# Performance work log

Measured on AMD Instinct MI355X. Metric: run time of the kernel, lower is better.

Reference implementation:

```python
import jax, jax.numpy as jnp
import numpy as np

D = 1024
DFF = 4096
B, S = 4, 2048
EPS = 1e-6
SLOPE = 0.01  # torch LeakyReLU default


def setup_inputs() -> dict:
    key = jax.random.key(0)
    ks = jax.random.split(key, 16)
    sd = 1.0 / np.sqrt(D)
    sf = 1.0 / np.sqrt(DFF)
    return {
        "X": jax.random.normal(ks[0], (B, S, D), dtype=jnp.float32),
        "intensity": jax.random.uniform(ks[1], (B, S, S), dtype=jnp.float32),
        "Wq": jax.random.uniform(ks[2], (D, D), jnp.float32, -sd, sd),
        "bq": jax.random.uniform(ks[3], (D,), jnp.float32, -sd, sd),
        "Wk": jax.random.uniform(ks[4], (D, D), jnp.float32, -sd, sd),
        "bk": jax.random.uniform(ks[5], (D,), jnp.float32, -sd, sd),
        "Wv": jax.random.uniform(ks[6], (D, D), jnp.float32, -sd, sd),
        "bv": jax.random.uniform(ks[7], (D,), jnp.float32, -sd, sd),
        "Wo": jax.random.uniform(ks[8], (D, D), jnp.float32, -sd, sd),
        "bo": jax.random.uniform(ks[9], (D,), jnp.float32, -sd, sd),
        "W1": jax.random.uniform(ks[10], (D, DFF), jnp.float32, -sd, sd),
        "b1": jax.random.uniform(ks[11], (DFF,), jnp.float32, -sd, sd),
        "W2": jax.random.uniform(ks[12], (DFF, D), jnp.float32, -sf, sf),
        "b2": jax.random.uniform(ks[13], (D,), jnp.float32, -sf, sf),
        "g1": jnp.ones((D,), jnp.float32),
        "be1": jnp.zeros((D,), jnp.float32),
        "g2": jnp.ones((D,), jnp.float32),
        "be2": jnp.zeros((D,), jnp.float32),
    }


def _layernorm(x, g, b):
    mu = jnp.mean(x, axis=-1, keepdims=True)
    var = jnp.mean(jnp.square(x - mu), axis=-1, keepdims=True)
    return (x - mu) * jax.lax.rsqrt(var + EPS) * g + b


def reference(X, intensity, Wq, bq, Wk, bk, Wv, bv, Wo, bo, W1, b1, W2, b2, g1, be1, g2, be2):
    d_k = X.shape[-1]
    q = X @ Wq + bq
    k = X @ Wk + bk
    v = X @ Wv + bv
    # scores: [B,S,S]; scale applied to k^T as in source
    scores = jnp.einsum('bid,bjd->bij', q, k) / jnp.sqrt(jnp.float32(d_k))
    attn = jax.nn.softmax(scores, axis=-1) + intensity  # post-softmax bias add
    out = jnp.einsum('bij,bjd->bid', attn, v) @ Wo + bo
    h = _layernorm(out + X, g1, be1)
    ffn = jax.nn.leaky_relu(h @ W1 + b1, negative_slope=SLOPE) @ W2 + b2
    return _layernorm(ffn + h, g2, be2)
```

## Files before the change

### kernel.cpp

```cpp
#include <hip/hip_runtime.h>

#define B_   4
#define S_   2048
#define D_   1024
#define DFF_ 4096

typedef __attribute__((ext_vector_type(8))) short short8;
typedef __attribute__((ext_vector_type(4))) float floatx4;

__device__ __forceinline__ unsigned short f2b(float f) {
    unsigned int u = __float_as_uint(f);
    unsigned int r = (u + 0x7fffu + ((u >> 16) & 1u)) >> 16;
    return (unsigned short)r;
}
__device__ __forceinline__ float b2f(unsigned short u) {
    return __uint_as_float((unsigned int)u << 16);
}

__device__ __forceinline__ void swizzle_xy(int gx, int gy, int& bx, int& by) {
    if ((gy & 7) == 0) {
        const int linear = by * gx + bx;
        const int xcd = linear & 7;
        const int slot = linear >> 3;
        const int r = slot / gx;
        by = xcd * (gy >> 3) + r;
        bx = slot - r * gx;
    }
}

#define GLL(src, dst) __builtin_amdgcn_global_load_lds( \
    (const __attribute__((address_space(1))) void*)(src), \
    (__attribute__((address_space(3))) void*)(dst), 16, 0, 0)

__device__ __forceinline__ void barrier_mem() {
    asm volatile("" ::: "memory");
    __builtin_amdgcn_s_barrier();
    asm volatile("" ::: "memory");
}

__device__ __forceinline__ void gemm_core256sq(
    const unsigned short* __restrict__ A,
    const unsigned short* __restrict__ Bt,
    int ldA, int ldB, int K, int m0, int n0,
    unsigned short* __restrict__ lds,
    floatx4 acc[8][4])
{
    const int tid  = threadIdx.x;
    const int lane = tid & 63;
    const int wave = tid >> 6;
    const int wm   = wave >> 2;
    const int wn   = wave & 3;

    const int ra = tid >> 3;
    const int pg = tid & 7;
    const int cg = (pg ^ (ra & 7)) * 8;
    const unsigned short* gA = A  + (long long)(m0 + ra) * ldA + cg;
    const unsigned short* gB = Bt + (long long)(n0 + ra) * ldB + cg;
    const long long rsA = 64LL * ldA;
    const long long rsB = 64LL * ldB;
    unsigned short* const sAbase = lds + wave * 512;
    unsigned short* const sBbase = lds + 32768 + wave * 512;

    const int fr = lane & 15;
    const int q  = lane >> 4;
    const int sw0 = (q ^ (fr & 7)) * 8;
    const int sw1 = sw0 ^ 32;
    const unsigned short* const pA = lds + (wm * 128 + fr) * 64;
    const unsigned short* const pB = lds + 32768 + (wn * 64 + fr) * 64;

    short8 Af[4][2];
    short8 Bf[2][2][2];

#define STG_A(buf, h, kk) do { \
    const unsigned short* _s = gA + (long long)(h) * 2 * rsA + (kk); \
    unsigned short* _d = sAbase + (buf) * 16384 + (h) * 8192; \
    GLL(_s, _d); GLL(_s + rsA, _d + 4096); } while (0)
#define STG_B(buf, h, kk) do { \
    const unsigned short* _s = gB + (long long)(h) * 2 * rsB + (kk); \
    unsigned short* _d = sBbase + (buf) * 16384 + (h) * 8192; \
    GLL(_s, _d); GLL(_s + rsB, _d + 4096); } while (0)
#define LD_A(bufo, mh) do { \
    _Pragma("unroll") for (int _i = 0; _i < 4; ++_i) { \
        Af[_i][0] = *(const short8*)(pA + (bufo) + (mh) * 4096 + _i * 1024 + sw0); \
        Af[_i][1] = *(const short8*)(pA + (bufo) + (mh) * 4096 + _i * 1024 + sw1); } } while (0)
#define LD_B(bufo, np) do { \
    _Pragma("unroll") for (int _j = 0; _j < 2; ++_j) { \
        Bf[np][_j][0] = *(const short8*)(pB + (bufo) + (np) * 2048 + _j * 1024 + sw0); \
        Bf[np][_j][1] = *(const short8*)(pB + (bufo) + (np) * 2048 + _j * 1024 + sw1); } } while (0)
#define MM(mh, np) do { \
    _Pragma("unroll") for (int _i = 0; _i < 4; ++_i) \
    _Pragma("unroll") for (int _j = 0; _j < 2; ++_j) \
    _Pragma("unroll") for (int _h = 0; _h < 2; ++_h) \
        acc[(mh) * 4 + _i][(np) * 2 + _j] = __builtin_amdgcn_mfma_f32_16x16x32_bf16( \
            Af[_i][_h], Bf[np][_j][_h], acc[(mh) * 4 + _i][(np) * 2 + _j], 0, 0, 0); \
    } while (0)
#define PRIO1() __builtin_amdgcn_s_setprio(1)
#define PRIO0() __builtin_amdgcn_s_setprio(0)
#define VMC(n)  asm volatile("s_waitcnt vmcnt(" #n ")" ::: "memory")

    const int NT = K >> 6;
    const long long kcap = (long long)K - 64;

    STG_B(0, 0, 0); STG_B(0, 1, 0);
    STG_A(0, 0, 0); STG_A(0, 1, 0);
    STG_B(1, 0, 64); STG_B(1, 1, 64);
    VMC(4);
    barrier_mem();

    for (int t = 0; t < NT; t += 2) {
        const long long k1 = (long long)(t + 1) * 64;
        long long k2 = (long long)(t + 2) * 64; if (k2 > kcap) k2 = kcap;
        long long k3 = (long long)(t + 3) * 64; if (k3 > kcap) k3 = kcap;

        STG_A(1, 0, k1); STG_A(1, 1, k1);
        LD_A(0, 0); LD_B(0, 0); LD_B(0, 1);
        PRIO1(); MM(0, 0); MM(0, 1); PRIO0();
        barrier_mem();
        STG_B(0, 0, k2); STG_B(0, 1, k2);
        LD_A(0, 1);
        PRIO1(); MM(1, 0); MM(1, 1); PRIO0();
        VMC(4);
        barrier_mem();
        STG_A(0, 0, k2); STG_A(0, 1, k2);
        LD_A(16384, 0); LD_B(16384, 0); LD_B(16384, 1);
        PRIO1(); MM(0, 0); MM(0, 1); PRIO0();
        barrier_mem();
        STG_B(1, 0, k3); STG_B(1, 1, k3);
        LD_A(16384, 1);
        PRIO1(); MM(1, 0); MM(1, 1); PRIO0();
        VMC(4);
        barrier_mem();
    }
    VMC(0);

#undef STG_A
#undef STG_B
#undef LD_A
#undef LD_B
#undef MM
#undef PRIO1
#undef PRIO0
#undef VMC
}

__global__ __launch_bounds__(256) void cast_bf16_kernel(
    const float4* __restrict__ src, ushort4* __restrict__ dst, int n4)
{
    int i = blockIdx.x * 256 + threadIdx.x;
    if (i < n4) {
        float4 f = src[i];
        ushort4 u;
        u.x = f2b(f.x); u.y = f2b(f.y); u.z = f2b(f.z); u.w = f2b(f.w);
        dst[i] = u;
    }
}

__global__ __launch_bounds__(256) void transpose_cast_kernel(
    const float* __restrict__ W, unsigned short* __restrict__ Wt, int K, int N)
{
    __shared__ float tile[32][33];
    const int tx = threadIdx.x;
    const int ty = threadIdx.y;
    const int bx = blockIdx.x * 32;
    const int by = blockIdx.y * 32;
#pragma unroll
    for (int j = 0; j < 32; j += 8)
        tile[ty + j][tx] = W[(long long)(by + ty + j) * N + bx + tx];
    __syncthreads();
#pragma unroll
    for (int j = 0; j < 32; j += 8)
        Wt[(long long)(bx + ty + j) * K + by + tx] = f2b(tile[tx][ty + j]);
}

__global__ __launch_bounds__(256) void vtrans_kernel(
    const unsigned short* __restrict__ Vb, unsigned short* __restrict__ Vt)
{
    __shared__ unsigned short tile[64][68];
    const int b  = blockIdx.z;
    const int s0 = blockIdx.y * 64;
    const int d0 = blockIdx.x * 64;
    const int tx = threadIdx.x & 15;
    const int ty = threadIdx.x >> 4;

    const unsigned short* src = Vb + ((long long)b * S_ + s0) * D_ + d0;
#pragma unroll
    for (int j = 0; j < 4; j++) {
        const int s = j * 16 + ty;
        ushort4 v = *(const ushort4*)(src + (long long)s * D_ + tx * 4);
        tile[tx * 4 + 0][s] = v.x;
        tile[tx * 4 + 1][s] = v.y;
        tile[tx * 4 + 2][s] = v.z;
        tile[tx * 4 + 3][s] = v.w;
    }
    __syncthreads();
    unsigned short* dst = Vt + ((long long)b * D_ + d0) * S_ + s0;
#pragma unroll
    for (int j = 0; j < 4; j++) {
        const int d = j * 16 + ty;
        ushort4 v;
        v.x = tile[d][tx * 4 + 0];
        v.y = tile[d][tx * 4 + 1];
        v.z = tile[d][tx * 4 + 2];
        v.w = tile[d][tx * 4 + 3];
        *(ushort4*)(dst + (long long)d * S_ + tx * 4) = v;
    }
}

template <int OUT_BF16, int ACT_LEAKY, int HAS_BIAS>
__global__ __launch_bounds__(512, 2) void gemm_bt(
    const unsigned short* __restrict__ A,
    const unsigned short* __restrict__ Bt,
    void* __restrict__ Cptr,
    const float* __restrict__ bias,
    int M, int N, int K, float scale,
    long long sA, long long sB, long long sC)
{
    __shared__ unsigned short lds[65536];

    const int lane = threadIdx.x & 63;
    const int wave = threadIdx.x >> 6;
    const int z    = blockIdx.z;

    int bx = blockIdx.x, by = blockIdx.y;
    swizzle_xy(gridDim.x, gridDim.y, bx, by);
    const int m0 = by * 256;
    const int n0 = bx * 256;

    floatx4 acc[8][4];
#pragma unroll
    for (int i = 0; i < 8; i++)
#pragma unroll
        for (int j = 0; j < 4; j++) acc[i][j] = floatx4{0.f, 0.f, 0.f, 0.f};

    gemm_core256sq(A + (long long)z * sA, Bt + (long long)z * sB,
                   K, K, K, m0, n0, lds, acc);

    const int wr = (wave >> 2) * 128;
    const int wc = (wave & 3) * 64;
    const int cr = (lane >> 4) * 4;
    const int cc = lane & 15;
    float* Cf = (float*)Cptr;
    unsigned short* Cb = (unsigned short*)Cptr;

#pragma unroll
    for (int mi = 0; mi < 8; mi++) {
#pragma unroll
        for (int ni = 0; ni < 4; ni++) {
            const int col = n0 + wc + ni * 16 + cc;
            const float bv = HAS_BIAS ? bias[col] : 0.0f;
#pragma unroll
            for (int r = 0; r < 4; r++) {
                const int row = m0 + wr + mi * 16 + cr + r;
                float v = acc[mi][ni][r] * scale + bv;
                if (ACT_LEAKY) v = (v > 0.0f) ? v : 0.01f * v;
                const long long idx = (long long)z * sC + (long long)row * N + col;
                if (OUT_BF16) Cb[idx] = f2b(v); else Cf[idx] = v;
            }
        }
    }
}

template <int NK>
__global__ __launch_bounds__(512, 2) void gemm_bt_sk(
    const unsigned short* __restrict__ A,
    const unsigned short* __restrict__ Bt,
    unsigned short* __restrict__ P,
    int M, int N, int Kslice, int ldA, int ldB,
    long long sA, long long sB)
{
    __shared__ unsigned short lds[65536];

    const int lane = threadIdx.x & 63;
    const int wave = threadIdx.x >> 6;
    const int z    = blockIdx.z;
    const int ks   = z % NK;
    const int b    = z / NK;
    const int nb   = gridDim.z / NK;

    int bx = blockIdx.x, by = blockIdx.y;
    swizzle_xy(gridDim.x, gridDim.y, bx, by);
    const int m0 = by * 256;
    const int n0 = bx * 256;

    floatx4 acc[8][4];
#pragma unroll
    for (int i = 0; i < 8; i++)
#pragma unroll
        for (int j = 0; j < 4; j++) acc[i][j] = floatx4{0.f, 0.f, 0.f, 0.f};

    gemm_core256sq(A + (long long)b * sA + (long long)ks * Kslice,
                   Bt + (long long)b * sB + (long long)ks * Kslice,
                   ldA, ldB, Kslice, m0, n0, lds, acc);

    const long long pbase = ((long long)ks * nb + b) * (long long)M * N;

    const int wr = (wave >> 2) * 128;
    const int wc = (wave & 3) * 64;
    const int cr = (lane >> 4) * 4;
    const int cc = lane & 15;

#pragma unroll
    for (int mi = 0; mi < 8; mi++) {
#pragma unroll
        for (int ni = 0; ni < 4; ni++) {
            const int col = n0 + wc + ni * 16 + cc;
#pragma unroll
            for (int r = 0; r < 4; r++) {
                const int row = m0 + wr + mi * 16 + cr + r;
                P[pbase + (long long)row * N + col] = f2b(acc[mi][ni][r]);
            }
        }
    }
}

__global__ __launch_bounds__(512, 2) void gemm_qkv(
    const unsigned short* __restrict__ A,
    const unsigned short* __restrict__ Bt,
    unsigned short* __restrict__ Qb,
    unsigned short* __restrict__ Kb,
    unsigned short* __restrict__ Vb,
    const float* __restrict__ bq,
    const float* __restrict__ bk,
    const float* __restrict__ bv)
{
    __shared__ unsigned short lds[65536];

    const int lane = threadIdx.x & 63;
    const int wave = threadIdx.x >> 6;

    int bx = blockIdx.x, by = blockIdx.y;
    swizzle_xy(gridDim.x, gridDim.y, bx, by);
    const int m0 = by * 256;
    const int n0 = bx * 256;

    floatx4 acc[8][4];
#pragma unroll
    for (int i = 0; i < 8; i++)
#pragma unroll
        for (int j = 0; j < 4; j++) acc[i][j] = floatx4{0.f, 0.f, 0.f, 0.f};

    gemm_core256sq(A, Bt, D_, D_, D_, m0, n0, lds, acc);

    const int wr = (wave >> 2) * 128;
    const int wc = (wave & 3) * 64;
    const int cr = (lane >> 4) * 4;
    const int cc = lane & 15;

#pragma unroll
    for (int mi = 0; mi < 8; mi++) {
#pragma unroll
        for (int ni = 0; ni < 4; ni++) {
            const int col = n0 + wc + ni * 16 + cc;
            const int seg = col >> 10;
            const int c = col & 1023;
            const float* bp = (seg == 0) ? bq : ((seg == 1) ? bk : bv);
            unsigned short* dp = (seg == 0) ? Qb : ((seg == 1) ? Kb : Vb);
            const float bval = bp[c];
#pragma unroll
            for (int r = 0; r < 4; r++) {
                const int row = m0 + wr + mi * 16 + cr + r;
                dp[(long long)row * D_ + c] = f2b(acc[mi][ni][r] + bval);
            }
        }
    }
}

__global__ __launch_bounds__(256) void avred_kernel(
    const ushort4* __restrict__ p0, const ushort4* __restrict__ p1,
    ushort4* __restrict__ dst, int n4)
{
    int i = blockIdx.x * 256 + threadIdx.x;
    if (i < n4) {
        ushort4 a = p0[i], b = p1[i];
        ushort4 u;
        u.x = f2b(b2f(a.x) + b2f(b.x)); u.y = f2b(b2f(a.y) + b2f(b.y));
        u.z = f2b(b2f(a.z) + b2f(b.z)); u.w = f2b(b2f(a.w) + b2f(b.w));
        dst[i] = u;
    }
}

template <int HAS_OUTB>
__global__ __launch_bounds__(256) void ln_red_kernel(
    const unsigned short* __restrict__ p0, const unsigned short* __restrict__ p1,
    const float* __restrict__ resid, const float* __restrict__ bias,
    const float* __restrict__ g, const float* __restrict__ b,
    float* __restrict__ out_f, unsigned short* __restrict__ out_b)
{
    __shared__ float red[8];
    const long long row = blockIdx.x;
    const int tid = threadIdx.x;
    const ushort4 a0 = ((const ushort4*)(p0 + row * D_))[tid];
    const ushort4 a1 = ((const ushort4*)(p1 + row * D_))[tid];
    const float4 rv = ((const float4*)(resid + row * D_))[tid];
    const float4 bi = ((const float4*)bias)[tid];
    float v0 = b2f(a0.x) + b2f(a1.x) + bi.x + rv.x;
    float v1 = b2f(a0.y) + b2f(a1.y) + bi.y + rv.y;
    float v2 = b2f(a0.z) + b2f(a1.z) + bi.z + rv.z;
    float v3 = b2f(a0.w) + b2f(a1.w) + bi.w + rv.w;

    float s = v0 + v1 + v2 + v3;
#pragma unroll
    for (int o = 32; o > 0; o >>= 1) s += __shfl_xor(s, o);
    if ((tid & 63) == 0) red[tid >> 6] = s;
    __syncthreads();
    const float mean = (red[0] + red[1] + red[2] + red[3]) * (1.0f / D_);

    const float d0 = v0 - mean, d1 = v1 - mean, d2 = v2 - mean, d3 = v3 - mean;
    float qv = d0 * d0 + d1 * d1 + d2 * d2 + d3 * d3;
#pragma unroll
    for (int o = 32; o > 0; o >>= 1) qv += __shfl_xor(qv, o);
    if ((tid & 63) == 0) red[4 + (tid >> 6)] = qv;
    __syncthreads();
    const float var = (red[4] + red[5] + red[6] + red[7]) * (1.0f / D_);
    const float inv = rsqrtf(var + 1e-6f);

    const float4 gv = ((const float4*)g)[tid];
    const float4 bv = ((const float4*)b)[tid];
    const float o0 = d0 * inv * gv.x + bv.x;
    const float o1 = d1 * inv * gv.y + bv.y;
    const float o2 = d2 * inv * gv.z + bv.z;
    const float o3 = d3 * inv * gv.w + bv.w;

    ((float4*)(out_f + row * D_))[tid] = float4{o0, o1, o2, o3};
    if (HAS_OUTB) {
        ushort4 u; u.x = f2b(o0); u.y = f2b(o1); u.z = f2b(o2); u.w = f2b(o3);
        ((ushort4*)(out_b + row * D_))[tid] = u;
    }
}

__global__ __launch_bounds__(256) void softmax_bias_kernel(
    const unsigned short* __restrict__ scores, const float* __restrict__ intensity,
    unsigned short* __restrict__ attn)
{
    __shared__ float red[8];
    const long long row = blockIdx.x;
    const int tid = threadIdx.x;
    const ushort4* s4 = (const ushort4*)(scores + row * S_);
    const float4* i4 = (const float4*)(intensity + row * S_);
    ushort4* dst = (ushort4*)(attn + row * S_);

    float vv[8];
    {
        ushort4 a = s4[tid], b = s4[tid + 256];
        vv[0] = b2f(a.x); vv[1] = b2f(a.y); vv[2] = b2f(a.z); vv[3] = b2f(a.w);
        vv[4] = b2f(b.x); vv[5] = b2f(b.y); vv[6] = b2f(b.z); vv[7] = b2f(b.w);
    }

    float mx = vv[0];
#pragma unroll
    for (int i = 1; i < 8; i++) mx = fmaxf(mx, vv[i]);
#pragma unroll
    for (int o = 32; o > 0; o >>= 1) mx = fmaxf(mx, __shfl_xor(mx, o));
    if ((tid & 63) == 0) red[tid >> 6] = mx;
    __syncthreads();
    mx = fmaxf(fmaxf(red[0], red[1]), fmaxf(red[2], red[3]));

    float e[8];
    float sum = 0.f;
#pragma unroll
    for (int i = 0; i < 8; i++) { e[i] = __expf(vv[i] - mx); sum += e[i]; }
#pragma unroll
    for (int o = 32; o > 0; o >>= 1) sum += __shfl_xor(sum, o);
    if ((tid & 63) == 0) red[4 + (tid >> 6)] = sum;
    __syncthreads();
    sum = red[4] + red[5] + red[6] + red[7];
    const float rs = 1.0f / sum;

#pragma unroll
    for (int i = 0; i < 2; i++) {
        float4 iv = i4[tid + 256 * i];
        ushort4 o;
        o.x = f2b(e[4 * i + 0] * rs + iv.x);
        o.y = f2b(e[4 * i + 1] * rs + iv.y);
        o.z = f2b(e[4 * i + 2] * rs + iv.z);
        o.w = f2b(e[4 * i + 3] * rs + iv.w);
        dst[tid + 256 * i] = o;
    }
}

extern "C" void kernel_launch(void* const* d_in, const int* in_sizes, int n_in,
                              void* d_out, int out_size, void* d_ws, size_t ws_size,
                              hipStream_t stream)
{
    const float* X   = (const float*)d_in[0];
    const float* inten = (const float*)d_in[1];
    const float* Wq  = (const float*)d_in[2];
    const float* bq  = (const float*)d_in[3];
    const float* Wk  = (const float*)d_in[4];
    const float* bk  = (const float*)d_in[5];
    const float* Wv  = (const float*)d_in[6];
    const float* bv  = (const float*)d_in[7];
    const float* Wo  = (const float*)d_in[8];
    const float* bo  = (const float*)d_in[9];
    const float* W1  = (const float*)d_in[10];
    const float* b1  = (const float*)d_in[11];
    const float* W2  = (const float*)d_in[12];
    const float* b2  = (const float*)d_in[13];
    const float* g1  = (const float*)d_in[14];
    const float* be1 = (const float*)d_in[15];
    const float* g2  = (const float*)d_in[16];
    const float* be2 = (const float*)d_in[17];
    float* out = (float*)d_out;

    char* ws = (char*)d_ws;
    const size_t MB = 1ull << 20;
    unsigned short* Xb   = (unsigned short*)(ws + 0);
    unsigned short* Wqkv = (unsigned short*)(ws + 16 * MB);
    unsigned short* Wot  = (unsigned short*)(ws + 22 * MB);
    unsigned short* W1t  = (unsigned short*)(ws + 24 * MB);
    unsigned short* W2t  = (unsigned short*)(ws + 32 * MB);
    unsigned short* Qb   = (unsigned short*)(ws + 40 * MB);
    unsigned short* Kb   = (unsigned short*)(ws + 56 * MB);
    unsigned short* Vt   = (unsigned short*)(ws + 72 * MB);
    unsigned short* Sc   = (unsigned short*)(ws + 88 * MB);
    unsigned short* Vb   = (unsigned short*)(ws + 152 * MB);
    unsigned short* At   = (unsigned short*)(ws + 152 * MB);
    unsigned short* AVp  = (unsigned short*)(ws + 88 * MB);
    unsigned short* AVb  = (unsigned short*)(ws + 0);
    unsigned short* Op   = (unsigned short*)(ws + 152 * MB);
    float*          Hf   = (float*)(ws + 40 * MB);
    unsigned short* Hb   = (unsigned short*)(ws + 72 * MB);
    unsigned short* F1   = (unsigned short*)(ws + 88 * MB);
    unsigned short* Fp   = (unsigned short*)(ws + 152 * MB);

    const dim3 blk(256);
    const dim3 blk512(512);
    const dim3 tblk(32, 8);
    const long long MN_d = (long long)B_ * S_ * D_;

    cast_bf16_kernel<<<dim3(8192), blk, 0, stream>>>(
        (const float4*)X, (ushort4*)Xb, B_ * S_ * D_ / 4);
    transpose_cast_kernel<<<dim3(D_ / 32, D_ / 32), tblk, 0, stream>>>(
        Wq, Wqkv, D_, D_);
    transpose_cast_kernel<<<dim3(D_ / 32, D_ / 32), tblk, 0, stream>>>(
        Wk, Wqkv + 1024 * 1024, D_, D_);
    transpose_cast_kernel<<<dim3(D_ / 32, D_ / 32), tblk, 0, stream>>>(
        Wv, Wqkv + 2048 * 1024, D_, D_);
    transpose_cast_kernel<<<dim3(D_ / 32, D_ / 32), tblk, 0, stream>>>(Wo, Wot, D_, D_);
    transpose_cast_kernel<<<dim3(DFF_ / 32, D_ / 32), tblk, 0, stream>>>(W1, W1t, D_, DFF_);
    transpose_cast_kernel<<<dim3(D_ / 32, DFF_ / 32), tblk, 0, stream>>>(W2, W2t, DFF_, D_);

    gemm_qkv<<<dim3(12, 32), blk512, 0, stream>>>(Xb, Wqkv, Qb, Kb, Vb, bq, bk, bv);

    vtrans_kernel<<<dim3(D_ / 64, S_ / 64, B_), blk, 0, stream>>>(Vb, Vt);

    gemm_bt<1, 0, 0><<<dim3(8, 8, 4), blk512, 0, stream>>>(
        Qb, Kb, Sc, nullptr, S_, S_, D_, 0.03125f,
        (long long)S_ * D_, (long long)S_ * D_, (long long)S_ * S_);

    softmax_bias_kernel<<<dim3(B_ * S_), blk, 0, stream>>>(Sc, inten, At);

    gemm_bt_sk<2><<<dim3(4, 8, 8), blk512, 0, stream>>>(
        At, Vt, AVp, S_, D_, S_ / 2, S_, S_,
        (long long)S_ * S_, (long long)D_ * S_);
    avred_kernel<<<dim3(8192), blk, 0, stream>>>(
        (const ushort4*)AVp, (const ushort4*)(AVp + MN_d), (ushort4*)AVb,
        (int)(MN_d / 4));

    gemm_bt_sk<2><<<dim3(4, 32, 2), blk512, 0, stream>>>(
        AVb, Wot, Op, B_ * S_, D_, D_ / 2, D_, D_, 0, 0);

    ln_red_kernel<1><<<dim3(B_ * S_), blk, 0, stream>>>(
        Op, Op + MN_d, X, bo, g1, be1, Hf, Hb);

    gemm_bt<1, 1, 1><<<dim3(16, 32), blk512, 0, stream>>>(
        Hb, W1t, F1, b1, B_ * S_, DFF_, D_, 1.0f, 0, 0, 0);

    gemm_bt_sk<2><<<dim3(4, 32, 2), blk512, 0, stream>>>(
        F1, W2t, Fp, B_ * S_, D_, DFF_ / 2, DFF_, DFF_, 0, 0);

    ln_red_kernel<0><<<dim3(B_ * S_), blk, 0, stream>>>(
        Fp, Fp + MN_d, Hf, b2, g2, be2, out, nullptr);
}
```

Before: 557.8 us.

## Restructure GEMM main loop into eight-phase ping-pong schedule with interleaved tile staging

The 256x256 bf16 GEMM core now runs eight smaller phases per two K-tiles instead of four. Each phase loads its own A/B fragments, issues one half-tile global-to-LDS stage, gates on LDS counters and a barrier, then runs 16 MFMAs. The row mapping is also changed: each wave now covers interleaved 64-row A blocks and 32-row B blocks, with matching new staging offsets. The aim is finer-grained overlap of global loads, LDS reads and MFMA work, and lower register pressure from short-lived fragments, at the cost of twice as many barriers.

New measurement: 594.6 us. 1.07x slower.

```diff
diff --git a/kernel.cpp b/kernel.cpp
--- a/kernel.cpp
+++ b/kernel.cpp
@@ -54,56 +54,63 @@
     const int ra = tid >> 3;
     const int pg = tid & 7;
     const int cg = (pg ^ (ra & 7)) * 8;
-    const unsigned short* gA = A  + (long long)(m0 + ra) * ldA + cg;
-    const unsigned short* gB = Bt + (long long)(n0 + ra) * ldB + cg;
-    const long long rsA = 64LL * ldA;
-    const long long rsB = 64LL * ldB;
-    unsigned short* const sAbase = lds + wave * 512;
-    unsigned short* const sBbase = lds + 32768 + wave * 512;
+    const unsigned short* gA = A + (long long)(m0 + ra) * ldA + cg;
+    const int brow = ((ra >> 5) << 6) + (ra & 31);
+    const unsigned short* gB = Bt + (long long)(n0 + brow) * ldB + cg;
+    const long long r64A = 64LL * ldA;
+    const long long r32B = 32LL * ldB;
+    unsigned short* const dA = lds + wave * 512;
+    unsigned short* const dB = lds + 32768 + wave * 512;
 
     const int fr = lane & 15;
     const int q  = lane >> 4;
     const int sw0 = (q ^ (fr & 7)) * 8;
     const int sw1 = sw0 ^ 32;
-    const unsigned short* const pA = lds + (wm * 128 + fr) * 64;
-    const unsigned short* const pB = lds + 32768 + (wn * 64 + fr) * 64;
-
-    short8 Af[4][2];
-    short8 Bf[2][2][2];
-
-#define STG_A(buf, h, kk) do { \
-    const unsigned short* _s = gA + (long long)(h) * 2 * rsA + (kk); \
-    unsigned short* _d = sAbase + (buf) * 16384 + (h) * 8192; \
-    GLL(_s, _d); GLL(_s + rsA, _d + 4096); } while (0)
-#define STG_B(buf, h, kk) do { \
-    const unsigned short* _s = gB + (long long)(h) * 2 * rsB + (kk); \
-    unsigned short* _d = sBbase + (buf) * 16384 + (h) * 8192; \
-    GLL(_s, _d); GLL(_s + rsB, _d + 4096); } while (0)
-#define LD_A(bufo, mh) do { \
+    const unsigned short* const pA0 = lds + (wm * 64 + fr) * 64;
+    const unsigned short* const pB0 = lds + 32768 + (wn * 32 + fr) * 64;
+
+#define STG_Aa(buf, kk) do { \
+    GLL(gA + (kk),            dA + (buf) * 16384 + 0); \
+    GLL(gA + 2 * r64A + (kk), dA + (buf) * 16384 + 4096); } while (0)
+#define STG_Ab(buf, kk) do { \
+    GLL(gA + r64A + (kk),     dA + (buf) * 16384 + 8192); \
+    GLL(gA + 3 * r64A + (kk), dA + (buf) * 16384 + 12288); } while (0)
+#define STG_Ba(buf, kk) do { \
+    GLL(gB + (kk),            dB + (buf) * 16384 + 0); \
+    GLL(gB + 4 * r32B + (kk), dB + (buf) * 16384 + 4096); } while (0)
+#define STG_Bb(buf, kk) do { \
+    GLL(gB + r32B + (kk),     dB + (buf) * 16384 + 8192); \
+    GLL(gB + 5 * r32B + (kk), dB + (buf) * 16384 + 12288); } while (0)
+#define VMC(n)  asm volatile("s_waitcnt vmcnt(" #n ")" ::: "memory")
+
+#define PHASE(bufo, mh, np, STAGE, GATE) do { \
+    short8 af[4][2], bf[2][2]; \
     _Pragma("unroll") for (int _i = 0; _i < 4; ++_i) { \
-        Af[_i][0] = *(const short8*)(pA + (bufo) + (mh) * 4096 + _i * 1024 + sw0); \
-        Af[_i][1] = *(const short8*)(pA + (bufo) + (mh) * 4096 + _i * 1024 + sw1); } } while (0)
-#define LD_B(bufo, np) do { \
+        af[_i][0] = *(const short8*)(pA0 + (bufo) + (mh) * 8192 + _i * 1024 + sw0); \
+        af[_i][1] = *(const short8*)(pA0 + (bufo) + (mh) * 8192 + _i * 1024 + sw1); } \
     _Pragma("unroll") for (int _j = 0; _j < 2; ++_j) { \
-        Bf[np][_j][0] = *(const short8*)(pB + (bufo) + (np) * 2048 + _j * 1024 + sw0); \
-        Bf[np][_j][1] = *(const short8*)(pB + (bufo) + (np) * 2048 + _j * 1024 + sw1); } } while (0)
-#define MM(mh, np) do { \
+        bf[_j][0] = *(const short8*)(pB0 + (bufo) + (np) * 8192 + _j * 1024 + sw0); \
+        bf[_j][1] = *(const short8*)(pB0 + (bufo) + (np) * 8192 + _j * 1024 + sw1); } \
+    STAGE; \
+    asm volatile("s_waitcnt lgkmcnt(8)" ::: "memory"); \
+    barrier_mem(); \
+    asm volatile("s_waitcnt lgkmcnt(0)" ::: "memory"); \
+    __builtin_amdgcn_s_setprio(1); \
     _Pragma("unroll") for (int _i = 0; _i < 4; ++_i) \
     _Pragma("unroll") for (int _j = 0; _j < 2; ++_j) \
     _Pragma("unroll") for (int _h = 0; _h < 2; ++_h) \
         acc[(mh) * 4 + _i][(np) * 2 + _j] = __builtin_amdgcn_mfma_f32_16x16x32_bf16( \
-            Af[_i][_h], Bf[np][_j][_h], acc[(mh) * 4 + _i][(np) * 2 + _j], 0, 0, 0); \
-    } while (0)
-#define PRIO1() __builtin_amdgcn_s_setprio(1)
-#define PRIO0() __builtin_amdgcn_s_setprio(0)
-#define VMC(n)  asm volatile("s_waitcnt vmcnt(" #n ")" ::: "memory")
+            af[_i][_h], bf[_j][_h], acc[(mh) * 4 + _i][(np) * 2 + _j], 0, 0, 0); \
+    __builtin_amdgcn_s_setprio(0); \
+    GATE; \
+    barrier_mem(); \
+} while (0)
 
     const int NT = K >> 6;
     const long long kcap = (long long)K - 64;
 
-    STG_B(0, 0, 0); STG_B(0, 1, 0);
-    STG_A(0, 0, 0); STG_A(0, 1, 0);
-    STG_B(1, 0, 64); STG_B(1, 1, 64);
+    STG_Aa(0, 0); STG_Ba(0, 0); STG_Ab(0, 0); STG_Bb(0, 0);
+    STG_Aa(1, 64); STG_Ba(1, 64);
     VMC(4);
     barrier_mem();
 
@@ -112,34 +119,22 @@
         long long k2 = (long long)(t + 2) * 64; if (k2 > kcap) k2 = kcap;
         long long k3 = (long long)(t + 3) * 64; if (k3 > kcap) k3 = kcap;
 
-        STG_A(1, 0, k1); STG_A(1, 1, k1);
-        LD_A(0, 0); LD_B(0, 0); LD_B(0, 1);
-        PRIO1(); MM(0, 0); MM(0, 1); PRIO0();
-        barrier_mem();
-        STG_B(0, 0, k2); STG_B(0, 1, k2);
-        LD_A(0, 1);
-        PRIO1(); MM(1, 0); MM(1, 1); PRIO0();
-        VMC(4);
-        barrier_mem();
-        STG_A(0, 0, k2); STG_A(0, 1, k2);
-        LD_A(16384, 0); LD_B(16384, 0); LD_B(16384, 1);
-        PRIO1(); MM(0, 0); MM(0, 1); PRIO0();
-        barrier_mem();
-        STG_B(1, 0, k3); STG_B(1, 1, k3);
-        LD_A(16384, 1);
-        PRIO1(); MM(1, 0); MM(1, 1); PRIO0();
-        VMC(4);
-        barrier_mem();
+        PHASE(0,     0, 0, STG_Ab(1, k1), ((void)0));
+        PHASE(0,     0, 1, STG_Bb(1, k1), ((void)0));
+        PHASE(0,     1, 0, STG_Aa(0, k2), ((void)0));
+        PHASE(0,     1, 1, STG_Ba(0, k2), VMC(4));
+        PHASE(16384, 0, 0, STG_Ab(0, k2), ((void)0));
+        PHASE(16384, 0, 1, STG_Bb(0, k2), ((void)0));
+        PHASE(16384, 1, 0, STG_Aa(1, k3), ((void)0));
+        PHASE(16384, 1, 1, STG_Ba(1, k3), VMC(4));
     }
     VMC(0);
 
-#undef STG_A
-#undef STG_B
-#undef LD_A
-#undef LD_B
-#undef MM
-#undef PRIO1
-#undef PRIO0
+#undef STG_Aa
+#undef STG_Ab
+#undef STG_Ba
+#undef STG_Bb
+#undef PHASE
 #undef VMC
 }
 
```
